# Kernel optimization log

Hardware: AMD Instinct MI355X
Metric: run time of the kernel (lower is better)

Reference implementation:

```python
import jax, jax.numpy as jnp
import numpy as np


def setup_inputs() -> dict:
    key = jax.random.key(0)
    k1, k2, k3, k4, k5, k6 = jax.random.split(key, 6)
    B, S, I, H = 64, 512, 1024, 1024
    scale_ih = 1.0 / np.sqrt(I)
    scale_hh = 1.0 / np.sqrt(H)
    return {
        "inputs": jax.random.normal(k1, (B, S, I), dtype=jnp.float32),
        "h0": jax.random.normal(k2, (1, B, H), dtype=jnp.float32),
        "weight_ih": jax.random.normal(k3, (H, I), dtype=jnp.float32) * scale_ih,
        "weight_hh": jax.random.normal(k4, (H, H), dtype=jnp.float32) * scale_hh,
        "bias_ih": jax.random.normal(k5, (H,), dtype=jnp.float32) * 0.01,
        "bias_hh": jax.random.normal(k6, (H,), dtype=jnp.float32) * 0.01,
    }


def reference(inputs, h0, weight_ih, weight_hh, bias_ih, bias_hh):
    # Elman RNN with ReLU: h_t = relu(x_t W_ih^T + b_ih + h_{t-1} W_hh^T + b_hh)
    # inputs: [B, S, I]; h0: [1, B, H]
    # Precompute the input projection for all timesteps in one big GEMM.
    x_proj = jnp.einsum('bsi,hi->bsh', inputs, weight_ih) + bias_ih + bias_hh  # [B,S,H]

    def step(h, xp_t):
        h_new = jax.nn.relu(xp_t + jnp.matmul(h, weight_hh.T))  # [B,H]
        return h_new, h_new

    h_init = h0[0]  # [B, H]
    h_last, outs = jax.lax.scan(step, h_init, jnp.swapaxes(x_proj, 0, 1))  # outs: [S,B,H]
    outputs = jnp.swapaxes(outs, 0, 1)  # [B, S, H]
    h_n = h_last[None]  # [1, B, H]
    return outputs, h_n
```

## Files before the change

kernel.cpp:

```cpp
#include <hip/hip_runtime.h>
#include <hip/hip_bf16.h>
#include <stdint.h>

#define BATCH 64
#define SEQ   512
#define INDIM 1024
#define HDIM  1024
#define NBLK  256
#define NGRP  8
#define GSLOT 32
#define FPAD  16
#define SLAB_BYTES 32768

typedef short bf16x8 __attribute__((ext_vector_type(8)));
typedef short s16x4  __attribute__((ext_vector_type(4)));
typedef float f32x2  __attribute__((ext_vector_type(2)));
typedef float f32x4  __attribute__((ext_vector_type(4)));
typedef unsigned short u16;
typedef unsigned int   u32;
typedef u32 u32x2 __attribute__((ext_vector_type(2)));
typedef u32 u32x4 __attribute__((ext_vector_type(4)));
typedef u16 u16x4 __attribute__((ext_vector_type(4)));

static __device__ __forceinline__ u16 f2bf(float x) {
  unsigned int u = __float_as_uint(x);
  u += 0x7fffu + ((u >> 16) & 1u);
  return (u16)(u >> 16);
}
static __device__ __forceinline__ float bf2f(u16 b) {
  return __uint_as_float(((unsigned int)b) << 16);
}

static __device__ __forceinline__ int coh_ld_i32(const int* p) {
  int v;
  asm volatile("global_load_dword %0, %1, off sc0 sc1\n\t"
               "s_waitcnt vmcnt(0)"
               : "=&v"(v) : "v"(p) : "memory");
  return v;
}

static __device__ __forceinline__ void split4(float4 v, u16x4& hi, u16x4& lo) {
  hi.x = f2bf(v.x); lo.x = f2bf(v.x - bf2f(hi.x));
  hi.y = f2bf(v.y); lo.y = f2bf(v.y - bf2f(hi.y));
  hi.z = f2bf(v.z); lo.z = f2bf(v.z - bf2f(hi.z));
  hi.w = f2bf(v.w); lo.w = f2bf(v.w - bf2f(hi.w));
}
static __device__ __forceinline__ bf16x8 ld8(const u16* p) {
  s16x4 a = *(const s16x4*)p;
  s16x4 b = *(const s16x4*)(p + 4);
  return __builtin_shufflevector(a, b, 0, 1, 2, 3, 4, 5, 6, 7);
}

__global__ void init0(int* __restrict__ flags, int n) {
  int i = blockIdx.x * blockDim.x + threadIdx.x;
  if (i < n) flags[i] = 0;
}

__global__ void init1(const float* __restrict__ h0, u32* __restrict__ hw) {
  int i = blockIdx.x * blockDim.x + threadIdx.x;
  if (i < BATCH * HDIM) {
    int b = i >> 10, k = i & 1023;
    int g = b >> 3, r = b & 7;
    int k32 = k >> 5, kg = (k >> 3) & 3, j = k & 7;
    float x = h0[i];
    u16 hi = f2bf(x);
    u16 lo = f2bf(x - bf2f(hi));
    size_t di = (size_t)g * (SLAB_BYTES / 4) + (size_t)(k32 * 256 + kg * 64 + r * 8 + j);
    hw[di] = (u32)hi | ((u32)lo << 16);
  }
}

__global__ __launch_bounds__(256) void xproj_kernel(const float* __restrict__ A,
                                                    const float* __restrict__ W,
                                                    const float* __restrict__ bih,
                                                    const float* __restrict__ bhh,
                                                    float* __restrict__ C) {
  __shared__ u16 Ah[4][128][12], Al[4][128][12], Bh[4][128][12], Bl[4][128][12];
  const int nb = blockIdx.x;
  const int mb = blockIdx.y;
  const int m_base = mb * 128, n_base = nb * 128;
  const int tid = (int)threadIdx.x;
  const int wid = tid >> 6, lane = tid & 63;
  const int wm = wid >> 1, wn = wid & 1;
  const int r = lane & 15, kg = lane >> 4;
  const int srow = tid >> 1;
  const int skq  = (tid & 1) * 16;

  const float* ap0 = A + (size_t)(m_base + srow) * INDIM + skq;
  const float* bp0 = W + (size_t)(n_base + srow) * INDIM + skq;

  f32x4 acc[4][4] = {};

  for (int k0 = 0; k0 < INDIM; k0 += 32) {
    float4 av[4], bv[4];
#pragma unroll
    for (int i = 0; i < 4; ++i) {
      av[i] = *(const float4*)(ap0 + k0 + i * 4);
      bv[i] = *(const float4*)(bp0 + k0 + i * 4);
    }
    __syncthreads();
#pragma unroll
    for (int i = 0; i < 4; ++i) {
      int kk = skq + i * 4;
      int kgw = kk >> 3, off = kk & 7;
      u16x4 hi, lo;
      split4(av[i], hi, lo);
      *(u16x4*)&Ah[kgw][srow][off] = hi;
      *(u16x4*)&Al[kgw][srow][off] = lo;
      split4(bv[i], hi, lo);
      *(u16x4*)&Bh[kgw][srow][off] = hi;
      *(u16x4*)&Bl[kgw][srow][off] = lo;
    }
    __syncthreads();

    bf16x8 ah[4], al[4], bhv[4], blv[4];
#pragma unroll
    for (int mf = 0; mf < 4; ++mf) {
      int row = wm * 64 + mf * 16 + r;
      ah[mf] = ld8(&Ah[kg][row][0]);
      al[mf] = ld8(&Al[kg][row][0]);
    }
#pragma unroll
    for (int nf = 0; nf < 4; ++nf) {
      int row = wn * 64 + nf * 16 + r;
      bhv[nf] = ld8(&Bh[kg][row][0]);
      blv[nf] = ld8(&Bl[kg][row][0]);
    }
#pragma unroll
    for (int mf = 0; mf < 4; ++mf)
#pragma unroll
      for (int nf = 0; nf < 4; ++nf) {
        acc[mf][nf] = __builtin_amdgcn_mfma_f32_16x16x32_bf16(ah[mf], bhv[nf], acc[mf][nf], 0, 0, 0);
        acc[mf][nf] = __builtin_amdgcn_mfma_f32_16x16x32_bf16(ah[mf], blv[nf], acc[mf][nf], 0, 0, 0);
        acc[mf][nf] = __builtin_amdgcn_mfma_f32_16x16x32_bf16(al[mf], bhv[nf], acc[mf][nf], 0, 0, 0);
      }
  }

#pragma unroll
  for (int nf = 0; nf < 4; ++nf) {
    int col = n_base + wn * 64 + nf * 16 + r;
    float bias = bih[col] + bhh[col];
#pragma unroll
    for (int mf = 0; mf < 4; ++mf) {
      int rowb = m_base + wm * 64 + mf * 16 + kg * 4;
#pragma unroll
      for (int q = 0; q < 4; ++q) {
        C[(size_t)(rowb + q) * HDIM + col] = acc[mf][nf][q] + bias;
      }
    }
  }
}

__global__ __launch_bounds__(512, 1) void rnn_scan(
    const float* __restrict__ Whh, float* __restrict__ out,
    char* ring, int* flags) {
  __shared__ u16 WH[32][2][64][8], WL[32][2][64][8];
  __shared__ __align__(16) float red[2][4][2][8][20];
  __shared__ __align__(8) float xfbuf[2][8][32];
  __shared__ __align__(8) float sbuf[2][8][32];

  const int blk = (int)blockIdx.x;
  const int grp = blk & 7;
  const int slot = blk >> 3;
  const int n0 = slot * 32;
  const int tid = (int)threadIdx.x;
  const int wv = tid >> 6, lane = tid & 63;

  for (int it = 0; it < 16; ++it) {
    int f4 = it * 512 + tid;
    int row = f4 >> 8;
    int k0 = (f4 & 255) * 4;
    float4 v = *(const float4*)(Whh + (size_t)(n0 + row) * HDIM + k0);
    int k32 = k0 >> 5, kgg = (k0 >> 3) & 3, j = k0 & 7;
    int nt = row >> 4, ln = kgg * 16 + (row & 15);
    u16x4 hi, lo;
    split4(v, hi, lo);
    *(u16x4*)&WH[k32][nt][ln][j] = hi;
    *(u16x4*)&WL[k32][nt][ln][j] = lo;
  }
  __syncthreads();

  char* const slab0 = ring + (size_t)grp * SLAB_BYTES;
  char* const slab1 = ring + (size_t)(NGRP + grp) * SLAB_BYTES;
  int* const gflag = flags + grp * (GSLOT * 2) * FPAD;

  const int r = lane & 15, kg = lane >> 4;
  const bool zrow = r >= 8;
  const int loff = wv * 8192 + kg * 256 + (r & 7) * 32;
  const int* const pollp = gflag + ((wv * 8 + ((lane >> 1) & 7)) * 2 + (lane & 1)) * FPAD;

  const int peid = (wv - 4) * 64 + lane;
  const int per = (peid >> 4) & 7;
  const int pec = (peid & 15) * 2;
  int* const myflag = gflag + (slot * 2 + (wv - 4)) * FPAD;

  const int qeid = (wv - 6) * 64 + lane;
  const int qer = (qeid >> 4) & 7;
  const int qec = (qeid & 15) * 2;
  float* const xpp = out + ((size_t)(grp * 8 + qer) * SEQ) * HDIM + n0 + qec;

  for (int t = 0; t <= SEQ; ++t) {
    if (wv < 4) {
      if (t < SEQ) {
        if (t > 0) {
          int v;
          do { v = coh_ld_i32(pollp); } while (!__all(v >= t));
        }
        u32x4 P0, P1, P2, P3, P4, P5, P6, P7, P8, P9, P10, P11, P12, P13, P14, P15;
        if (!zrow) {
          const char* b0 = ((t & 1) ? slab1 : slab0) + loff;
          const char* b1 = b0 + 4096;
          asm volatile(
              "global_load_dwordx4 %0, %8, off sc0 sc1\n\t"
              "global_load_dwordx4 %1, %8, off offset:16 sc0 sc1\n\t"
              "global_load_dwordx4 %2, %8, off offset:1024 sc0 sc1\n\t"
              "global_load_dwordx4 %3, %8, off offset:1040 sc0 sc1\n\t"
              "global_load_dwordx4 %4, %8, off offset:2048 sc0 sc1\n\t"
              "global_load_dwordx4 %5, %8, off offset:2064 sc0 sc1\n\t"
              "global_load_dwordx4 %6, %8, off offset:3072 sc0 sc1\n\t"
              "global_load_dwordx4 %7, %8, off offset:3088 sc0 sc1"
              : "=&v"(P0), "=&v"(P1), "=&v"(P2), "=&v"(P3),
                "=&v"(P4), "=&v"(P5), "=&v"(P6), "=&v"(P7)
              : "v"(b0) : "memory");
          asm volatile(
              "global_load_dwordx4 %0, %8, off sc0 sc1\n\t"
              "global_load_dwordx4 %1, %8, off offset:16 sc0 sc1\n\t"
              "global_load_dwordx4 %2, %8, off offset:1024 sc0 sc1\n\t"
              "global_load_dwordx4 %3, %8, off offset:1040 sc0 sc1\n\t"
              "global_load_dwordx4 %4, %8, off offset:2048 sc0 sc1\n\t"
              "global_load_dwordx4 %5, %8, off offset:2064 sc0 sc1\n\t"
              "global_load_dwordx4 %6, %8, off offset:3072 sc0 sc1\n\t"
              "global_load_dwordx4 %7, %8, off offset:3088 sc0 sc1"
              : "=&v"(P8), "=&v"(P9), "=&v"(P10), "=&v"(P11),
                "=&v"(P12), "=&v"(P13), "=&v"(P14), "=&v"(P15)
              : "v"(b1) : "memory");
          asm volatile("s_waitcnt vmcnt(0)"
              : "+v"(P0), "+v"(P1), "+v"(P2), "+v"(P3),
                "+v"(P4), "+v"(P5), "+v"(P6), "+v"(P7),
                "+v"(P8), "+v"(P9), "+v"(P10), "+v"(P11),
                "+v"(P12), "+v"(P13), "+v"(P14), "+v"(P15));
        } else {
          P0 = P1 = P2 = P3 = P4 = P5 = P6 = P7 = (u32x4){0, 0, 0, 0};
          P8 = P9 = P10 = P11 = P12 = P13 = P14 = P15 = (u32x4){0, 0, 0, 0};
        }

        f32x4 acc0 = {0.f, 0.f, 0.f, 0.f};
        f32x4 acc1 = {0.f, 0.f, 0.f, 0.f};
#define DO_K32(i, QA, QB)                                                      \
        {                                                                      \
          u32 d0 = QA[0], d1 = QA[1], d2 = QA[2], d3 = QA[3];                  \
          u32 d4 = QB[0], d5 = QB[1], d6 = QB[2], d7 = QB[3];                  \
          union { u32 w[4]; bf16x8 v; } AH, AL;                                \
          AH.w[0] = (d0 & 0xFFFFu) | (d1 << 16);                               \
          AH.w[1] = (d2 & 0xFFFFu) | (d3 << 16);                               \
          AH.w[2] = (d4 & 0xFFFFu) | (d5 << 16);                               \
          AH.w[3] = (d6 & 0xFFFFu) | (d7 << 16);                               \
          AL.w[0] = (d0 >> 16) | (d1 & 0xFFFF0000u);                           \
          AL.w[1] = (d2 >> 16) | (d3 & 0xFFFF0000u);                           \
          AL.w[2] = (d4 >> 16) | (d5 & 0xFFFF0000u);                           \
          AL.w[3] = (d6 >> 16) | (d7 & 0xFFFF0000u);                           \
          int k32 = wv * 8 + (i);                                              \
          bf16x8 b0h = *(const bf16x8*)&WH[k32][0][lane][0];                   \
          bf16x8 b0l = *(const bf16x8*)&WL[k32][0][lane][0];                   \
          bf16x8 b1h = *(const bf16x8*)&WH[k32][1][lane][0];                   \
          bf16x8 b1l = *(const bf16x8*)&WL[k32][1][lane][0];                   \
          acc0 = __builtin_amdgcn_mfma_f32_16x16x32_bf16(AH.v, b0h, acc0, 0, 0, 0); \
          acc0 = __builtin_amdgcn_mfma_f32_16x16x32_bf16(AH.v, b0l, acc0, 0, 0, 0); \
          acc0 = __builtin_amdgcn_mfma_f32_16x16x32_bf16(AL.v, b0h, acc0, 0, 0, 0); \
          acc1 = __builtin_amdgcn_mfma_f32_16x16x32_bf16(AH.v, b1h, acc1, 0, 0, 0); \
          acc1 = __builtin_amdgcn_mfma_f32_16x16x32_bf16(AH.v, b1l, acc1, 0, 0, 0); \
          acc1 = __builtin_amdgcn_mfma_f32_16x16x32_bf16(AL.v, b1h, acc1, 0, 0, 0); \
        }
        DO_K32(0, P0, P1)
        DO_K32(1, P2, P3)
        DO_K32(2, P4, P5)
        DO_K32(3, P6, P7)
        DO_K32(4, P8, P9)
        DO_K32(5, P10, P11)
        DO_K32(6, P12, P13)
        DO_K32(7, P14, P15)
#undef DO_K32

        if (kg < 2) {
#pragma unroll
          for (int q = 0; q < 4; ++q) {
            red[t & 1][wv][0][kg * 4 + q][r] = acc0[q];
            red[t & 1][wv][1][kg * 4 + q][r] = acc1[q];
          }
        }
      }
    } else if (wv < 6) {
      if (t >= 1) {
        const int ph = (t - 1) & 1;
        f32x2 s = *(const f32x2*)&xfbuf[ph][per][pec];
        const int nt = pec >> 4, c = pec & 15;
#pragma unroll
        for (int w = 0; w < 4; ++w) s += *(const f32x2*)&red[ph][w][nt][per][c];
        s.x = s.x > 0.f ? s.x : 0.f;
        s.y = s.y > 0.f ? s.y : 0.f;
        *(f32x2*)&sbuf[ph][per][pec] = s;
        u16 h0 = f2bf(s.x), h1 = f2bf(s.y);
        u16 l0 = f2bf(s.x - bf2f(h0)), l1 = f2bf(s.y - bf2f(h1));
        u32x2 D = {(u32)h0 | ((u32)l0 << 16), (u32)h1 | ((u32)l1 << 16)};
        char* hp = ((t & 1) ? slab1 : slab0) +
                   (size_t)(slot * 1024 + (pec >> 3) * 256 + per * 32 + (pec & 7) * 4);
        asm volatile("global_store_dwordx2 %0, %1, off sc1\n\t"
                     "s_waitcnt vmcnt(0)"
                     :: "v"(hp), "v"(D) : "memory");
        if (lane == 0) {
          int tv = t;
          asm volatile("global_store_dword %0, %1, off sc0 sc1"
                       :: "v"(myflag), "v"(tv) : "memory");
        }
      }
    } else {
      if (t >= 2) {
        f32x2 sv = *(const f32x2*)&sbuf[t & 1][qer][qec];
        __builtin_nontemporal_store(sv, (f32x2*)(xpp + (size_t)(t - 2) * HDIM));
      }
      if (t < SEQ) {
        f32x2 xv = *(const f32x2*)(xpp + (size_t)t * HDIM);
        *(f32x2*)&xfbuf[t & 1][qer][qec] = xv;
      }
    }
    __syncthreads();
  }

  if (wv >= 6) {
    f32x2 sv = *(const f32x2*)&sbuf[(SEQ - 1) & 1][qer][qec];
    __builtin_nontemporal_store(sv, (f32x2*)(xpp + (size_t)(SEQ - 1) * HDIM));
  }
}

__global__ void copy_hn(const float* __restrict__ out, float* __restrict__ hn) {
  int idx = blockIdx.x * blockDim.x + threadIdx.x;
  if (idx < BATCH * HDIM) {
    int b = idx >> 10, j = idx & 1023;
    hn[idx] = out[((size_t)b * SEQ + (SEQ - 1)) * (size_t)HDIM + j];
  }
}

extern "C" void kernel_launch(void* const* d_in, const int* in_sizes, int n_in,
                              void* d_out, int out_size, void* d_ws, size_t ws_size,
                              hipStream_t stream) {
  const float* inputs = (const float*)d_in[0];
  const float* h0     = (const float*)d_in[1];
  const float* w_ih   = (const float*)d_in[2];
  const float* w_hh   = (const float*)d_in[3];
  const float* b_ih   = (const float*)d_in[4];
  const float* b_hh   = (const float*)d_in[5];

  float* outBase = (float*)d_out;
  float* hnBase  = outBase + (size_t)BATCH * SEQ * HDIM;

  char* ring = (char*)d_ws;
  int* flags = (int*)(ring + (size_t)2 * NGRP * SLAB_BYTES);
  const int nflags = NGRP * GSLOT * 2 * FPAD;

  init0<<<(nflags + 255) / 256, 256, 0, stream>>>(flags, nflags);
  init1<<<(BATCH * HDIM + 255) / 256, 256, 0, stream>>>(h0, (u32*)ring);

  xproj_kernel<<<dim3(8, 256), 256, 0, stream>>>(inputs, w_ih, b_ih, b_hh, outBase);

  const float* wha = w_hh;
  float* oa = outBase;
  char* ra = ring;
  int* fa = flags;
  void* args[4] = {&wha, &oa, &ra, &fa};
  (void)hipLaunchCooperativeKernel((const void*)rnn_scan, dim3(NBLK), dim3(512), args, 0, stream);

  copy_hn<<<256, 256, 0, stream>>>(outBase, hnBase);
}
```

Baseline: 1.877 ms.

## Repartition RNN scan to 128 blocks each serving four batch groups

The persistent recurrent scan moves from 256 blocks (8 batch groups × 32 column slots of 32 outputs) to 128 blocks of 576 threads. Each block now owns 16 output columns and processes four batch groups in sequence inside every timestep. Eight waves split K for the MFMA, and a ninth wave handles x_proj prefetch and output stores. The intent is to halve the cross-block flag and polling fan-in, and to interleave groups so the global sync latency of one group overlaps work on the others. The cost is one __syncthreads per group per step, fewer blocks on the GPU, and single-wave reductions.

```diff
diff --git a/kernel.cpp b/kernel.cpp
--- a/kernel.cpp
+++ b/kernel.cpp
@@ -6,11 +6,11 @@
 #define SEQ   512
 #define INDIM 1024
 #define HDIM  1024
-#define NBLK  256
+#define NBLK  128
 #define NGRP  8
-#define GSLOT 32
+#define GSLOT 64
 #define FPAD  16
-#define SLAB_BYTES 32768
+#define SLAB_DW 8192
 
 typedef short bf16x8 __attribute__((ext_vector_type(8)));
 typedef short s16x4  __attribute__((ext_vector_type(4)));
@@ -65,7 +65,7 @@
     float x = h0[i];
     u16 hi = f2bf(x);
     u16 lo = f2bf(x - bf2f(hi));
-    size_t di = (size_t)g * (SLAB_BYTES / 4) + (size_t)(k32 * 256 + kg * 64 + r * 8 + j);
+    size_t di = (size_t)(g * 2) * SLAB_DW + (size_t)(k32 * 256 + (kg * 8 + r) * 8 + j);
     hw[di] = (u32)hi | ((u32)lo << 16);
   }
 }
@@ -151,65 +151,63 @@
   }
 }
 
-__global__ __launch_bounds__(512, 1) void rnn_scan(
+__global__ __launch_bounds__(576, 1) void rnn_scan(
     const float* __restrict__ Whh, float* __restrict__ out,
-    char* ring, int* flags) {
-  __shared__ u16 WH[32][2][64][8], WL[32][2][64][8];
-  __shared__ __align__(16) float red[2][4][2][8][20];
-  __shared__ __align__(8) float xfbuf[2][8][32];
-  __shared__ __align__(8) float sbuf[2][8][32];
+    u32* ring, int* flags) {
+  __shared__ u16 WH[32][64][8], WL[32][64][8];
+  __shared__ __align__(16) float red[4][8][8][18];
+  __shared__ __align__(8) float xfbuf[4][2][8][16];
+  __shared__ __align__(8) float sbuf[4][2][8][16];
 
   const int blk = (int)blockIdx.x;
-  const int grp = blk & 7;
-  const int slot = blk >> 3;
-  const int n0 = slot * 32;
+  const int q = blk >> 6;
+  const int slot = blk & 63;
+  const int n0 = slot * 16;
   const int tid = (int)threadIdx.x;
   const int wv = tid >> 6, lane = tid & 63;
-
-  for (int it = 0; it < 16; ++it) {
-    int f4 = it * 512 + tid;
+  const int r = lane & 15, kg = lane >> 4;
+  const bool zrow = r >= 8;
+
+  for (int f4 = tid; f4 < 4096; f4 += 576) {
     int row = f4 >> 8;
     int k0 = (f4 & 255) * 4;
     float4 v = *(const float4*)(Whh + (size_t)(n0 + row) * HDIM + k0);
-    int k32 = k0 >> 5, kgg = (k0 >> 3) & 3, j = k0 & 7;
-    int nt = row >> 4, ln = kgg * 16 + (row & 15);
+    int k32 = k0 >> 5, kgg = (k0 >> 3) & 3, jj = k0 & 7;
+    int ln = kgg * 16 + row;
     u16x4 hi, lo;
     split4(v, hi, lo);
-    *(u16x4*)&WH[k32][nt][ln][j] = hi;
-    *(u16x4*)&WL[k32][nt][ln][j] = lo;
+    *(u16x4*)&WH[k32][ln][jj] = hi;
+    *(u16x4*)&WL[k32][ln][jj] = lo;
+  }
+
+  const int er = lane >> 3;
+  const int ec = (lane & 7) * 2;
+
+  if (wv == 8) {
+#pragma unroll
+    for (int j = 0; j < 4; ++j) {
+      int g = q * 4 + j;
+      f32x2 xv = *(const f32x2*)(out + ((size_t)(g * 8 + er) * SEQ) * HDIM + n0 + ec);
+      *(f32x2*)&xfbuf[j][0][er][ec] = xv;
+    }
   }
   __syncthreads();
 
-  char* const slab0 = ring + (size_t)grp * SLAB_BYTES;
-  char* const slab1 = ring + (size_t)(NGRP + grp) * SLAB_BYTES;
-  int* const gflag = flags + grp * (GSLOT * 2) * FPAD;
-
-  const int r = lane & 15, kg = lane >> 4;
-  const bool zrow = r >= 8;
-  const int loff = wv * 8192 + kg * 256 + (r & 7) * 32;
-  const int* const pollp = gflag + ((wv * 8 + ((lane >> 1) & 7)) * 2 + (lane & 1)) * FPAD;
-
-  const int peid = (wv - 4) * 64 + lane;
-  const int per = (peid >> 4) & 7;
-  const int pec = (peid & 15) * 2;
-  int* const myflag = gflag + (slot * 2 + (wv - 4)) * FPAD;
-
-  const int qeid = (wv - 6) * 64 + lane;
-  const int qer = (qeid >> 4) & 7;
-  const int qec = (qeid & 15) * 2;
-  float* const xpp = out + ((size_t)(grp * 8 + qer) * SEQ) * HDIM + n0 + qec;
-
-  for (int t = 0; t <= SEQ; ++t) {
-    if (wv < 4) {
-      if (t < SEQ) {
+  for (int t = 0; t < SEQ; ++t) {
+    const int pb = t & 1;
+#pragma unroll
+    for (int j = 0; j < 4; ++j) {
+      const int g = q * 4 + j;
+      if (wv < 8) {
         if (t > 0) {
+          const int* fp = flags + (g * GSLOT + lane) * FPAD;
           int v;
-          do { v = coh_ld_i32(pollp); } while (!__all(v >= t));
-        }
-        u32x4 P0, P1, P2, P3, P4, P5, P6, P7, P8, P9, P10, P11, P12, P13, P14, P15;
+          do { v = coh_ld_i32(fp); } while (!__all(v >= t));
+        }
+        u32x4 P0, P1, P2, P3, P4, P5, P6, P7;
         if (!zrow) {
-          const char* b0 = ((t & 1) ? slab1 : slab0) + loff;
-          const char* b1 = b0 + 4096;
+          const char* a0 = (const char*)(ring + (size_t)(g * 2 + pb) * SLAB_DW)
+                           + (size_t)(wv * 4096 + (kg * 8 + r) * 32);
           asm volatile(
               "global_load_dwordx4 %0, %8, off sc0 sc1\n\t"
               "global_load_dwordx4 %1, %8, off offset:16 sc0 sc1\n\t"
@@ -221,31 +219,16 @@
               "global_load_dwordx4 %7, %8, off offset:3088 sc0 sc1"
               : "=&v"(P0), "=&v"(P1), "=&v"(P2), "=&v"(P3),
                 "=&v"(P4), "=&v"(P5), "=&v"(P6), "=&v"(P7)
-              : "v"(b0) : "memory");
-          asm volatile(
-              "global_load_dwordx4 %0, %8, off sc0 sc1\n\t"
-              "global_load_dwordx4 %1, %8, off offset:16 sc0 sc1\n\t"
-              "global_load_dwordx4 %2, %8, off offset:1024 sc0 sc1\n\t"
-              "global_load_dwordx4 %3, %8, off offset:1040 sc0 sc1\n\t"
-              "global_load_dwordx4 %4, %8, off offset:2048 sc0 sc1\n\t"
-              "global_load_dwordx4 %5, %8, off offset:2064 sc0 sc1\n\t"
-              "global_load_dwordx4 %6, %8, off offset:3072 sc0 sc1\n\t"
-              "global_load_dwordx4 %7, %8, off offset:3088 sc0 sc1"
-              : "=&v"(P8), "=&v"(P9), "=&v"(P10), "=&v"(P11),
-                "=&v"(P12), "=&v"(P13), "=&v"(P14), "=&v"(P15)
-              : "v"(b1) : "memory");
+              : "v"(a0)
+              : "memory");
           asm volatile("s_waitcnt vmcnt(0)"
               : "+v"(P0), "+v"(P1), "+v"(P2), "+v"(P3),
-                "+v"(P4), "+v"(P5), "+v"(P6), "+v"(P7),
-                "+v"(P8), "+v"(P9), "+v"(P10), "+v"(P11),
-                "+v"(P12), "+v"(P13), "+v"(P14), "+v"(P15));
+                "+v"(P4), "+v"(P5), "+v"(P6), "+v"(P7));
         } else {
           P0 = P1 = P2 = P3 = P4 = P5 = P6 = P7 = (u32x4){0, 0, 0, 0};
-          P8 = P9 = P10 = P11 = P12 = P13 = P14 = P15 = (u32x4){0, 0, 0, 0};
-        }
-
-        f32x4 acc0 = {0.f, 0.f, 0.f, 0.f};
-        f32x4 acc1 = {0.f, 0.f, 0.f, 0.f};
+        }
+
+        f32x4 acc = {0.f, 0.f, 0.f, 0.f};
 #define DO_K32(i, QA, QB)                                                      \
         {                                                                      \
           u32 d0 = QA[0], d1 = QA[1], d2 = QA[2], d3 = QA[3];                  \
@@ -259,76 +242,78 @@
           AL.w[1] = (d2 >> 16) | (d3 & 0xFFFF0000u);                           \
           AL.w[2] = (d4 >> 16) | (d5 & 0xFFFF0000u);                           \
           AL.w[3] = (d6 >> 16) | (d7 & 0xFFFF0000u);                           \
-          int k32 = wv * 8 + (i);                                              \
-          bf16x8 b0h = *(const bf16x8*)&WH[k32][0][lane][0];                   \
-          bf16x8 b0l = *(const bf16x8*)&WL[k32][0][lane][0];                   \
-          bf16x8 b1h = *(const bf16x8*)&WH[k32][1][lane][0];                   \
-          bf16x8 b1l = *(const bf16x8*)&WL[k32][1][lane][0];                   \
-          acc0 = __builtin_amdgcn_mfma_f32_16x16x32_bf16(AH.v, b0h, acc0, 0, 0, 0); \
-          acc0 = __builtin_amdgcn_mfma_f32_16x16x32_bf16(AH.v, b0l, acc0, 0, 0, 0); \
-          acc0 = __builtin_amdgcn_mfma_f32_16x16x32_bf16(AL.v, b0h, acc0, 0, 0, 0); \
-          acc1 = __builtin_amdgcn_mfma_f32_16x16x32_bf16(AH.v, b1h, acc1, 0, 0, 0); \
-          acc1 = __builtin_amdgcn_mfma_f32_16x16x32_bf16(AH.v, b1l, acc1, 0, 0, 0); \
-          acc1 = __builtin_amdgcn_mfma_f32_16x16x32_bf16(AL.v, b1h, acc1, 0, 0, 0); \
+          int k32 = wv * 4 + (i);                                              \
+          bf16x8 bh = *(const bf16x8*)&WH[k32][lane][0];                       \
+          bf16x8 bl = *(const bf16x8*)&WL[k32][lane][0];                       \
+          acc = __builtin_amdgcn_mfma_f32_16x16x32_bf16(AH.v, bh, acc, 0, 0, 0); \
+          acc = __builtin_amdgcn_mfma_f32_16x16x32_bf16(AH.v, bl, acc, 0, 0, 0); \
+          acc = __builtin_amdgcn_mfma_f32_16x16x32_bf16(AL.v, bh, acc, 0, 0, 0); \
         }
         DO_K32(0, P0, P1)
         DO_K32(1, P2, P3)
         DO_K32(2, P4, P5)
         DO_K32(3, P6, P7)
-        DO_K32(4, P8, P9)
-        DO_K32(5, P10, P11)
-        DO_K32(6, P12, P13)
-        DO_K32(7, P14, P15)
 #undef DO_K32
 
         if (kg < 2) {
 #pragma unroll
-          for (int q = 0; q < 4; ++q) {
-            red[t & 1][wv][0][kg * 4 + q][r] = acc0[q];
-            red[t & 1][wv][1][kg * 4 + q][r] = acc1[q];
-          }
+          for (int qq = 0; qq < 4; ++qq) red[j][wv][kg * 4 + qq][r] = acc[qq];
+        }
+      } else {
+        if (t >= 2) {
+          f32x2 sv = *(const f32x2*)&sbuf[j][pb][er][ec];
+          __builtin_nontemporal_store(sv,
+              (f32x2*)(out + ((size_t)(g * 8 + er) * SEQ + (t - 2)) * HDIM + n0 + ec));
+        }
+        if (t + 1 < SEQ) {
+          f32x2 xv = *(const f32x2*)(out + ((size_t)(g * 8 + er) * SEQ + (t + 1)) * HDIM + n0 + ec);
+          *(f32x2*)&xfbuf[j][pb ^ 1][er][ec] = xv;
         }
       }
-    } else if (wv < 6) {
-      if (t >= 1) {
-        const int ph = (t - 1) & 1;
-        f32x2 s = *(const f32x2*)&xfbuf[ph][per][pec];
-        const int nt = pec >> 4, c = pec & 15;
-#pragma unroll
-        for (int w = 0; w < 4; ++w) s += *(const f32x2*)&red[ph][w][nt][per][c];
+      __syncthreads();
+
+      if (wv == j) {
+        f32x2 s = *(const f32x2*)&xfbuf[j][pb][er][ec];
+#pragma unroll
+        for (int w = 0; w < 8; ++w) {
+          s.x += red[j][w][er][ec];
+          s.y += red[j][w][er][ec + 1];
+        }
         s.x = s.x > 0.f ? s.x : 0.f;
         s.y = s.y > 0.f ? s.y : 0.f;
-        *(f32x2*)&sbuf[ph][per][pec] = s;
+        *(f32x2*)&sbuf[j][pb][er][ec] = s;
+
         u16 h0 = f2bf(s.x), h1 = f2bf(s.y);
         u16 l0 = f2bf(s.x - bf2f(h0)), l1 = f2bf(s.y - bf2f(h1));
         u32x2 D = {(u32)h0 | ((u32)l0 << 16), (u32)h1 | ((u32)l1 << 16)};
-        char* hp = ((t & 1) ? slab1 : slab0) +
-                   (size_t)(slot * 1024 + (pec >> 3) * 256 + per * 32 + (pec & 7) * 4);
+        int cg = n0 + ec;
+        u32* hp = ring + (size_t)(g * 2 + (pb ^ 1)) * SLAB_DW
+                  + (size_t)((cg >> 5) * 256 + (((cg >> 3) & 3) * 8 + er) * 8 + (cg & 7));
         asm volatile("global_store_dwordx2 %0, %1, off sc1\n\t"
                      "s_waitcnt vmcnt(0)"
                      :: "v"(hp), "v"(D) : "memory");
         if (lane == 0) {
-          int tv = t;
+          int* fp = flags + (g * GSLOT + slot) * FPAD;
+          int tv = t + 1;
           asm volatile("global_store_dword %0, %1, off sc0 sc1"
-                       :: "v"(myflag), "v"(tv) : "memory");
+                       :: "v"(fp), "v"(tv) : "memory");
         }
       }
-    } else {
-      if (t >= 2) {
-        f32x2 sv = *(const f32x2*)&sbuf[t & 1][qer][qec];
-        __builtin_nontemporal_store(sv, (f32x2*)(xpp + (size_t)(t - 2) * HDIM));
-      }
-      if (t < SEQ) {
-        f32x2 xv = *(const f32x2*)(xpp + (size_t)t * HDIM);
-        *(f32x2*)&xfbuf[t & 1][qer][qec] = xv;
-      }
-    }
-    __syncthreads();
-  }
-
-  if (wv >= 6) {
-    f32x2 sv = *(const f32x2*)&sbuf[(SEQ - 1) & 1][qer][qec];
-    __builtin_nontemporal_store(sv, (f32x2*)(xpp + (size_t)(SEQ - 1) * HDIM));
+    }
+  }
+
+  __syncthreads();
+  if (wv == 8) {
+#pragma unroll
+    for (int j = 0; j < 4; ++j) {
+      int g = q * 4 + j;
+      f32x2 a = *(const f32x2*)&sbuf[j][(SEQ - 2) & 1][er][ec];
+      __builtin_nontemporal_store(a,
+          (f32x2*)(out + ((size_t)(g * 8 + er) * SEQ + (SEQ - 2)) * HDIM + n0 + ec));
+      f32x2 b = *(const f32x2*)&sbuf[j][(SEQ - 1) & 1][er][ec];
+      __builtin_nontemporal_store(b,
+          (f32x2*)(out + ((size_t)(g * 8 + er) * SEQ + (SEQ - 1)) * HDIM + n0 + ec));
+    }
   }
 }
 
@@ -353,21 +338,21 @@
   float* outBase = (float*)d_out;
   float* hnBase  = outBase + (size_t)BATCH * SEQ * HDIM;
 
-  char* ring = (char*)d_ws;
-  int* flags = (int*)(ring + (size_t)2 * NGRP * SLAB_BYTES);
-  const int nflags = NGRP * GSLOT * 2 * FPAD;
+  u32* ring = (u32*)d_ws;
+  int* flags = (int*)(ring + (size_t)NGRP * 2 * SLAB_DW);
+  const int nflags = NGRP * GSLOT * FPAD;
 
   init0<<<(nflags + 255) / 256, 256, 0, stream>>>(flags, nflags);
-  init1<<<(BATCH * HDIM + 255) / 256, 256, 0, stream>>>(h0, (u32*)ring);
+  init1<<<(BATCH * HDIM + 255) / 256, 256, 0, stream>>>(h0, ring);
 
   xproj_kernel<<<dim3(8, 256), 256, 0, stream>>>(inputs, w_ih, b_ih, b_hh, outBase);
 
   const float* wha = w_hh;
   float* oa = outBase;
-  char* ra = ring;
+  u32* ra = ring;
   int* fa = flags;
   void* args[4] = {&wha, &oa, &ra, &fa};
-  (void)hipLaunchCooperativeKernel((const void*)rnn_scan, dim3(NBLK), dim3(512), args, 0, stream);
+  (void)hipLaunchCooperativeKernel((const void*)rnn_scan, dim3(NBLK), dim3(576), args, 0, stream);
 
   copy_hn<<<256, 256, 0, stream>>>(outBase, hnBase);
 }
```

Result: slower. 4.312 ms (+129.7%).
